# Performance work log

Measured on AMD Instinct MI355X. Metric: run time of the kernel, lower is better.

The kernel has to match this reference:

```python
import jax, jax.numpy as jnp
import numpy as np

B, S, F, H, O = 256, 512, 64, 1024, 24  # batch, seq_len, input_size, hidden_size, output_size


def setup_inputs() -> dict:
    key = jax.random.key(0)
    ks = jax.random.split(key, 11)
    s = 1.0 / np.sqrt(H)  # PyTorch LSTM/Linear uniform init bound
    u = lambda k, shape: jax.random.uniform(k, shape, jnp.float32, -s, s)
    return {
        "x": jax.random.normal(ks[0], (B, S, F), jnp.float32),
        # layer 0 (gate order: i, f, g, o stacked along first dim)
        "W_ih0": u(ks[1], (4 * H, F)),
        "W_hh0": u(ks[2], (4 * H, H)),
        "b_ih0": u(ks[3], (4 * H,)),
        "b_hh0": u(ks[4], (4 * H,)),
        # layer 1
        "W_ih1": u(ks[5], (4 * H, H)),
        "W_hh1": u(ks[6], (4 * H, H)),
        "b_ih1": u(ks[7], (4 * H,)),
        "b_hh1": u(ks[8], (4 * H,)),
        # final projection over all timesteps: [O, H*S]
        "fc_W": jax.random.uniform(ks[9], (O, H * S), jnp.float32, -1.0 / np.sqrt(H * S), 1.0 / np.sqrt(H * S)),
        "fc_b": jax.random.uniform(ks[10], (O,), jnp.float32, -1.0 / np.sqrt(H * S), 1.0 / np.sqrt(H * S)),
    }


def _lstm_layer(x_sbf, W_ih, W_hh, b_ih, b_hh):
    # x_sbf: [S, B, Fin]; returns all hidden states [S, B, H]
    Hh = W_hh.shape[1]
    # precompute input contribution for all steps (one big GEMM)
    xg = jnp.einsum('sbf,gf->sbg', x_sbf, W_ih) + b_ih + b_hh  # [S, B, 4H]

    def step(carry, xg_t):
        h, c = carry
        gates = xg_t + h @ W_hh.T  # [B, 4H]
        i, f, g, o = jnp.split(gates, 4, axis=-1)
        c = jax.nn.sigmoid(f) * c + jax.nn.sigmoid(i) * jnp.tanh(g)
        h = jax.nn.sigmoid(o) * jnp.tanh(c)
        return (h, c), h

    h0 = jnp.zeros((x_sbf.shape[1], Hh), x_sbf.dtype)
    _, hs = jax.lax.scan(step, (h0, h0), xg)
    return hs  # [S, B, H]


def reference(x, W_ih0, W_hh0, b_ih0, b_hh0, W_ih1, W_hh1, b_ih1, b_hh1, fc_W, fc_b):
    xs = jnp.swapaxes(x, 0, 1)  # [S, B, F]
    h1 = _lstm_layer(xs, W_ih0, W_hh0, b_ih0, b_hh0)  # [S, B, H]
    h2 = _lstm_layer(h1, W_ih1, W_hh1, b_ih1, b_hh1)  # [S, B, H]
    # use_all_h=True: reshape [B, S, H] -> [B, S*H], then Linear
    flat = jnp.swapaxes(h2, 0, 1).reshape(x.shape[0], -1)
    return flat @ fc_W.T + fc_b  # [B, O]
```

## Files before the change

kernel.cpp:

```cpp
#include <hip/hip_runtime.h>
#include <hip/hip_fp16.h>

#define B_ 256
#define S_ 512
#define F_ 64
#define H_ 1024
#define O_ 24
#define G_ 4096
#define NT_ 64

typedef _Float16 half_t;
typedef _Float16 h8 __attribute__((ext_vector_type(8)));
typedef float f4 __attribute__((ext_vector_type(4)));

#define OFF_H1 ((size_t)0)
#define OFF_H2 (OFF_H1 + (size_t)2*B_*H_*2)
#define OFF_C1 (OFF_H2 + (size_t)2*B_*H_*2)
#define OFF_C2 (OFF_C1 + (size_t)B_*H_*4)
#define OFF_OP (OFF_C2 + (size_t)B_*H_*4)
#define ZBYTES (OFF_OP + (size_t)NT_*B_*O_*4)
#define OFF_BIAS0 (ZBYTES)
#define OFF_BIAS1 (OFF_BIAS0 + (size_t)G_*4)
#define OFF_XH    (OFF_BIAS1 + (size_t)G_*4)
#define OFF_WIH0  (OFF_XH + (size_t)B_*S_*F_*2)
#define OFF_WHH0  (OFF_WIH0 + (size_t)G_*F_*2)
#define OFF_WIH1  (OFF_WHH0 + (size_t)G_*H_*2)
#define OFF_WHH1  (OFF_WIH1 + (size_t)G_*H_*2)
#define WS_NEEDED (OFF_WHH1 + (size_t)G_*H_*2)

__global__ void k_bias(const float* __restrict__ bi0, const float* __restrict__ bh0,
                       const float* __restrict__ bi1, const float* __restrict__ bh1,
                       float* __restrict__ bias0, float* __restrict__ bias1) {
    int i = blockIdx.x * blockDim.x + threadIdx.x;
    if (i < G_) { bias0[i] = bi0[i] + bh0[i]; bias1[i] = bi1[i] + bh1[i]; }
}

__global__ void k_cvt(const float* __restrict__ src, half_t* __restrict__ dst, int n) {
    int i = blockIdx.x * blockDim.x + threadIdx.x;
    int stride = gridDim.x * blockDim.x;
    for (; i < n; i += stride) dst[i] = (half_t)src[i];
}

__global__ void k_pack(const float* __restrict__ src, half_t* __restrict__ dst, int NC) {
    int i = blockIdx.x * blockDim.x + threadIdx.x;
    int total = 32768 * NC;
    if (i >= total) return;
    int lane = i & 63;
    int j    = (i >> 6) & 3;
    int ck   = (i >> 8) % NC;
    int gh   = i / (256 * NC);
    int srow = (gh >> 5) * H_ + (gh & 31) * 32 + (j >> 1) * 16 + (lane & 15);
    int scol = ck * 64 + (j & 1) * 32 + (lane >> 4) * 8;
    const float* s = src + (size_t)srow * (NC * 64) + scol;
    h8 v;
    #pragma unroll
    for (int e = 0; e < 8; ++e) v[e] = (half_t)s[e];
    *(h8*)&dst[(size_t)i * 8] = v;
}

__device__ __forceinline__ void run_part(
    const int thr, const int bt, const int htp,
    const int cx, const int nchunks,
    const half_t* __restrict__ xb, const int ldx,
    const half_t* __restrict__ hp,
    const half_t* __restrict__ Wih, const half_t* __restrict__ Whh,
    const float* __restrict__ bias,
    float* __restrict__ c, half_t* __restrict__ hn_out,
    const float* __restrict__ fcWt, float* __restrict__ out_part,
    half_t* A_s, float* gate_s, float* h_s, float* fcw_s,
    const bool do_fc)
{
    const int wave = thr >> 6, lane = thr & 63;
    const int gate = wave >> 1, mh = wave & 1;
    const int quad = lane >> 4, l15 = lane & 15;
    const int ar = thr >> 3;
    const int ak = (thr & 7) * 8;
    const int ghW = gate * 32 + (htp >> 1);
    const int jo  = (htp & 1) * 2;

    float bv = bias[gate * H_ + htp * 16 + l15];
    f4 acc0 = (f4){bv, bv, bv, bv};
    f4 acc1 = acc0;

    auto loadA = [&](int ck) -> f4 {
        const half_t* Ab; int lda, k0;
        if (ck < cx) { Ab = xb; lda = ldx; k0 = ck * 64; }
        else         { Ab = hp; lda = H_;  k0 = (ck - cx) * 64; }
        return *(const f4*)&Ab[(size_t)(bt * 64 + ar) * lda + k0 + ak];
    };
    auto fetchW = [&](int ck, h8& r0, h8& r1) {
        const half_t* Wb; int ckk, NC;
        if (ck < cx) { Wb = Wih; ckk = ck;      NC = cx; }
        else         { Wb = Whh; ckk = ck - cx; NC = 16; }
        const half_t* base = Wb + ((size_t)(((ghW * NC) + ckk) * 4 + jo) * 64 + lane) * 8;
        r0 = *(const h8*)(base + 0 * 512);
        r1 = *(const h8*)(base + 1 * 512);
    };

    h8 W0a,W0b, W1a,W1b, W2a,W2b, W3a,W3b;
    f4 p0, p1, p2, p3;
    p0 = loadA(0); p1 = loadA(1); p2 = loadA(2); p3 = loadA(3);
    fetchW(0, W0a, W0b);
    fetchW(1, W1a, W1b);
    fetchW(2, W2a, W2b);

    const int eb = thr >> 4, ecol = thr & 15;
    const size_t cbase = (size_t)(bt * 64 + eb) * H_ + htp * 16 + ecol;
    float cpre0 = c[cbase];
    float cpre1 = c[cbase + (size_t)32 * H_];
    float fpre = 0.f;
    if (do_fc && thr < 384)
        fpre = fcWt[(size_t)(thr >> 4) * (S_ * H_) + htp * 16 + (thr & 15)];

    *(f4*)&A_s[0 * 4608 + ar * 72 + ak] = p0;
    *(f4*)&A_s[1 * 4608 + ar * 72 + ak] = p1;
    *(f4*)&A_s[2 * 4608 + ar * 72 + ak] = p2;
    *(f4*)&A_s[3 * 4608 + ar * 72 + ak] = p3;
    __syncthreads();

    for (int s = 0; s < nchunks; s += 4) {
        const int rem = nchunks - s;
        const int ns = rem < 4 ? rem : 4;
        int ns2 = rem - 4; if (ns2 < 0) ns2 = 0; if (ns2 > 4) ns2 = 4;
        const int bufo = ((s >> 2) & 1) * 18432;
        const int obuf = 18432 - bufo;

        if (ns2 > 0) p0 = loadA(s + 4);
        if (ns2 > 1) p1 = loadA(s + 5);
        if (ns2 > 2) p2 = loadA(s + 6);
        if (ns2 > 3) p3 = loadA(s + 7);

        #define STEP(i, C0,C1, N0,N1)                                                          \
        if (i < ns) {                                                                          \
            if (s + i + 3 < nchunks) fetchW(s + i + 3, N0, N1);                                \
            h8 a0 = *(const h8*)&A_s[bufo + i * 4608 + (mh * 32 + l15) * 72 + quad * 8];       \
            h8 a1 = *(const h8*)&A_s[bufo + i * 4608 + (mh * 32 + 16 + l15) * 72 + quad * 8];  \
            h8 a2 = *(const h8*)&A_s[bufo + i * 4608 + (mh * 32 + l15) * 72 + 32 + quad * 8];  \
            h8 a3 = *(const h8*)&A_s[bufo + i * 4608 + (mh * 32 + 16 + l15) * 72 + 32 + quad * 8]; \
            acc0 = __builtin_amdgcn_mfma_f32_16x16x32_f16(a0, C0, acc0, 0, 0, 0);              \
            acc1 = __builtin_amdgcn_mfma_f32_16x16x32_f16(a1, C0, acc1, 0, 0, 0);              \
            acc0 = __builtin_amdgcn_mfma_f32_16x16x32_f16(a2, C1, acc0, 0, 0, 0);              \
            acc1 = __builtin_amdgcn_mfma_f32_16x16x32_f16(a3, C1, acc1, 0, 0, 0);              \
        }
        STEP(0, W0a,W0b, W3a,W3b)
        STEP(1, W1a,W1b, W0a,W0b)
        STEP(2, W2a,W2b, W1a,W1b)
        STEP(3, W3a,W3b, W2a,W2b)
        #undef STEP

        if (ns2 > 0) {
                   *(f4*)&A_s[obuf + 0 * 4608 + ar * 72 + ak] = p0;
            if (ns2 > 1)     *(f4*)&A_s[obuf + 1 * 4608 + ar * 72 + ak] = p1;
            if (ns2 > 2)     *(f4*)&A_s[obuf + 2 * 4608 + ar * 72 + ak] = p2;
            if (ns2 > 3)     *(f4*)&A_s[obuf + 3 * 4608 + ar * 72 + ak] = p3;
            __syncthreads();
        }
    }
    __syncthreads();

    #pragma unroll
    for (int r = 0; r < 4; ++r) {
        gate_s[gate * (64 * 17) + (mh * 32 + quad * 4 + r) * 17 + l15]      = acc0[r];
        gate_s[gate * (64 * 17) + (mh * 32 + 16 + quad * 4 + r) * 17 + l15] = acc1[r];
    }
    __syncthreads();

    #pragma unroll
    for (int kk = 0; kk < 2; ++kk) {
        int b = eb + kk * 32;
        float gi = gate_s[0 * (64 * 17) + b * 17 + ecol];
        float gf = gate_s[1 * (64 * 17) + b * 17 + ecol];
        float gg = gate_s[2 * (64 * 17) + b * 17 + ecol];
        float go = gate_s[3 * (64 * 17) + b * 17 + ecol];
        float si = 1.f / (1.f + __expf(-gi));
        float sf = 1.f / (1.f + __expf(-gf));
        float so = 1.f / (1.f + __expf(-go));
        float tg = tanhf(gg);
        float cn = sf * (kk ? cpre1 : cpre0) + si * tg;
        size_t cidx = cbase + (size_t)kk * 32 * H_;
        c[cidx] = cn;
        float hnv = so * tanhf(cn);
        hn_out[cidx] = (half_t)hnv;
        if (do_fc) h_s[b * 17 + ecol] = hnv;
    }

    if (do_fc) {
        if (thr < 384) fcw_s[thr] = fpre;
        __syncthreads();
        #pragma unroll
        for (int q = 0; q < 3; ++q) {
            int p = thr + q * 512;
            int o = p >> 6, bb = p & 63;
            float s2 = 0.f;
            #pragma unroll
            for (int j = 0; j < 16; ++j)
                s2 += h_s[bb * 17 + j] * fcw_s[o * 16 + j];
            out_part[(size_t)htp * (B_ * O_) + (bt * 64 + bb) * O_ + o] += s2;
        }
    }
    __syncthreads();
}

__global__ __launch_bounds__(512, 2)
void k_phase(int t,
             const half_t* __restrict__ x_h,
             const half_t* __restrict__ Wih0, const half_t* __restrict__ Whh0,
             const float* __restrict__ bias0, float* __restrict__ c1g, half_t* __restrict__ h1buf,
             const half_t* __restrict__ Wih1, const half_t* __restrict__ Whh1,
             const float* __restrict__ bias1, float* __restrict__ c2g, half_t* __restrict__ h2buf,
             const float* __restrict__ fcW, float* __restrict__ out_part)
{
    __shared__ __align__(16) char smraw[73728];
    half_t* A_s    = (half_t*)smraw;
    float*  gate_s = (float*)smraw;
    float*  h_s    = (float*)(smraw + 17408);
    float*  fcw_s  = (float*)(smraw + 21760);

    const int n   = blockIdx.x;
    const int htp = (n & 7) + 8 * ((n >> 3) & 7);
    const int bt  = (n >> 6) & 3;
    const int thr = threadIdx.x;

    if (t < S_) {
        const int tt = t;
        run_part(thr, bt, htp, 1, 17,
                 x_h + (size_t)tt * F_, S_ * F_,
                 h1buf + (size_t)((tt - 1) & 1) * B_ * H_,
                 Wih0, Whh0, bias0, c1g,
                 h1buf + (size_t)(tt & 1) * B_ * H_,
                 nullptr, nullptr,
                 A_s, gate_s, h_s, fcw_s, false);
    }
    if (t > 0) {
        const int tt = t - 1;
        run_part(thr, bt, htp, 16, 32,
                 h1buf + (size_t)(tt & 1) * B_ * H_, H_,
                 h2buf + (size_t)((tt - 1) & 1) * B_ * H_,
                 Wih1, Whh1, bias1, c2g,
                 h2buf + (size_t)(tt & 1) * B_ * H_,
                 fcW + (size_t)tt * H_, out_part,
                 A_s, gate_s, h_s, fcw_s, true);
    }
}

__global__ void k_final(const float* __restrict__ out_part, const float* __restrict__ fcb,
                        float* __restrict__ out) {
    int i = blockIdx.x * blockDim.x + threadIdx.x;
    if (i >= B_ * O_) return;
    int o = i % O_;
    float s = fcb[o];
    for (int tl = 0; tl < NT_; ++tl) s += out_part[(size_t)tl * (B_ * O_) + i];
    out[i] = s;
}

extern "C" void kernel_launch(void* const* d_in, const int* in_sizes, int n_in,
                              void* d_out, int out_size, void* d_ws, size_t ws_size,
                              hipStream_t stream) {
    const float* x    = (const float*)d_in[0];
    const float* Wih0 = (const float*)d_in[1];
    const float* Whh0 = (const float*)d_in[2];
    const float* bih0 = (const float*)d_in[3];
    const float* bhh0 = (const float*)d_in[4];
    const float* Wih1 = (const float*)d_in[5];
    const float* Whh1 = (const float*)d_in[6];
    const float* bih1 = (const float*)d_in[7];
    const float* bhh1 = (const float*)d_in[8];
    const float* fcW  = (const float*)d_in[9];
    const float* fcb  = (const float*)d_in[10];

    char* ws = (char*)d_ws;
    half_t* h1buf  = (half_t*)(ws + OFF_H1);
    half_t* h2buf  = (half_t*)(ws + OFF_H2);
    float*  c1     = (float*)(ws + OFF_C1);
    float*  c2     = (float*)(ws + OFF_C2);
    float*  opart  = (float*)(ws + OFF_OP);
    float*  bias0  = (float*)(ws + OFF_BIAS0);
    float*  bias1  = (float*)(ws + OFF_BIAS1);
    half_t* x_h    = (half_t*)(ws + OFF_XH);
    half_t* wih0_p = (half_t*)(ws + OFF_WIH0);
    half_t* whh0_p = (half_t*)(ws + OFF_WHH0);
    half_t* wih1_p = (half_t*)(ws + OFF_WIH1);
    half_t* whh1_p = (half_t*)(ws + OFF_WHH1);

    hipMemsetAsync(d_ws, 0, ZBYTES, stream);

    k_bias<<<dim3((G_ + 255) / 256), dim3(256), 0, stream>>>(bih0, bhh0, bih1, bhh1, bias0, bias1);
    k_cvt<<<dim3(2048), dim3(256), 0, stream>>>(x, x_h, B_ * S_ * F_);
    k_pack<<<dim3(128),  dim3(256), 0, stream>>>(Wih0, wih0_p, 1);
    k_pack<<<dim3(2048), dim3(256), 0, stream>>>(Whh0, whh0_p, 16);
    k_pack<<<dim3(2048), dim3(256), 0, stream>>>(Wih1, wih1_p, 16);
    k_pack<<<dim3(2048), dim3(256), 0, stream>>>(Whh1, whh1_p, 16);

    dim3 grid(256), blk(512);
    for (int t = 0; t <= S_; ++t) {
        k_phase<<<grid, blk, 0, stream>>>(t, x_h,
                                          wih0_p, whh0_p, bias0, c1, h1buf,
                                          wih1_p, whh1_p, bias1, c2, h2buf,
                                          fcW, opart);
    }
    k_final<<<dim3((B_ * O_ + 255) / 256), dim3(256), 0, stream>>>(opart, fcb, (float*)d_out);
}
```

Before: 9.640 ms.

## Deepen K-loop prefetch to 8 chunks with doubled weight register pipeline

Restructures the per-step GEMM loop to process 8 K-chunks per iteration. It keeps 7 weight chunks in flight in registers instead of 3, and prefetches A tiles 8 to 12 chunks ahead into two LDS half-buffers. The goal is to hide more global-memory latency in the latency-bound recurrent step. In exchange it roughly doubles the register use for weights and prefetched A, which risks spills or lower occupancy.

```diff
diff --git a/kernel.cpp b/kernel.cpp
--- a/kernel.cpp
+++ b/kernel.cpp
@@ -97,12 +97,20 @@
         r1 = *(const h8*)(base + 1 * 512);
     };
 
-    h8 W0a,W0b, W1a,W1b, W2a,W2b, W3a,W3b;
+    h8 Ws0a,Ws0b, Ws1a,Ws1b, Ws2a,Ws2b, Ws3a,Ws3b,
+       Ws4a,Ws4b, Ws5a,Ws5b, Ws6a,Ws6b, Ws7a{},Ws7b{};
     f4 p0, p1, p2, p3;
-    p0 = loadA(0); p1 = loadA(1); p2 = loadA(2); p3 = loadA(3);
-    fetchW(0, W0a, W0b);
-    fetchW(1, W1a, W1b);
-    fetchW(2, W2a, W2b);
+    f4 q0, q1, q2, q3;
+
+    f4 a0_ = loadA(0), a1_ = loadA(1), a2_ = loadA(2), a3_ = loadA(3);
+    p0 = loadA(4); p1 = loadA(5); p2 = loadA(6); p3 = loadA(7);
+    fetchW(0, Ws0a, Ws0b);
+    fetchW(1, Ws1a, Ws1b);
+    fetchW(2, Ws2a, Ws2b);
+    fetchW(3, Ws3a, Ws3b);
+    fetchW(4, Ws4a, Ws4b);
+    fetchW(5, Ws5a, Ws5b);
+    fetchW(6, Ws6a, Ws6b);
 
     const int eb = thr >> 4, ecol = thr & 15;
     const size_t cbase = (size_t)(bt * 64 + eb) * H_ + htp * 16 + ecol;
@@ -112,51 +120,61 @@
     if (do_fc && thr < 384)
         fpre = fcWt[(size_t)(thr >> 4) * (S_ * H_) + htp * 16 + (thr & 15)];
 
-    *(f4*)&A_s[0 * 4608 + ar * 72 + ak] = p0;
-    *(f4*)&A_s[1 * 4608 + ar * 72 + ak] = p1;
-    *(f4*)&A_s[2 * 4608 + ar * 72 + ak] = p2;
-    *(f4*)&A_s[3 * 4608 + ar * 72 + ak] = p3;
+    *(f4*)&A_s[0 * 4608 + ar * 72 + ak] = a0_;
+    *(f4*)&A_s[1 * 4608 + ar * 72 + ak] = a1_;
+    *(f4*)&A_s[2 * 4608 + ar * 72 + ak] = a2_;
+    *(f4*)&A_s[3 * 4608 + ar * 72 + ak] = a3_;
     __syncthreads();
 
-    for (int s = 0; s < nchunks; s += 4) {
-        const int rem = nchunks - s;
-        const int ns = rem < 4 ? rem : 4;
-        int ns2 = rem - 4; if (ns2 < 0) ns2 = 0; if (ns2 > 4) ns2 = 4;
-        const int bufo = ((s >> 2) & 1) * 18432;
-        const int obuf = 18432 - bufo;
-
-        if (ns2 > 0) p0 = loadA(s + 4);
-        if (ns2 > 1) p1 = loadA(s + 5);
-        if (ns2 > 2) p2 = loadA(s + 6);
-        if (ns2 > 3) p3 = loadA(s + 7);
-
-        #define STEP(i, C0,C1, N0,N1)                                                          \
-        if (i < ns) {                                                                          \
-            if (s + i + 3 < nchunks) fetchW(s + i + 3, N0, N1);                                \
-            h8 a0 = *(const h8*)&A_s[bufo + i * 4608 + (mh * 32 + l15) * 72 + quad * 8];       \
-            h8 a1 = *(const h8*)&A_s[bufo + i * 4608 + (mh * 32 + 16 + l15) * 72 + quad * 8];  \
-            h8 a2 = *(const h8*)&A_s[bufo + i * 4608 + (mh * 32 + l15) * 72 + 32 + quad * 8];  \
-            h8 a3 = *(const h8*)&A_s[bufo + i * 4608 + (mh * 32 + 16 + l15) * 72 + 32 + quad * 8]; \
-            acc0 = __builtin_amdgcn_mfma_f32_16x16x32_f16(a0, C0, acc0, 0, 0, 0);              \
-            acc1 = __builtin_amdgcn_mfma_f32_16x16x32_f16(a1, C0, acc1, 0, 0, 0);              \
-            acc0 = __builtin_amdgcn_mfma_f32_16x16x32_f16(a2, C1, acc0, 0, 0, 0);              \
-            acc1 = __builtin_amdgcn_mfma_f32_16x16x32_f16(a3, C1, acc1, 0, 0, 0);              \
+    for (int s = 0; s < nchunks; s += 8) {
+        if (s + 8  < nchunks) q0 = loadA(s + 8);
+        if (s + 9  < nchunks) q1 = loadA(s + 9);
+        if (s + 10 < nchunks) q2 = loadA(s + 10);
+        if (s + 11 < nchunks) q3 = loadA(s + 11);
+
+        #define STEP(i, C0,C1, N0,N1)                                                            \
+        if (s + i < nchunks) {                                                                   \
+            if (s + i + 7 < nchunks) fetchW(s + i + 7, N0, N1);                                  \
+            const int bo = (i) < 4 ? 0 : 18432;                                                  \
+            const int ii = (i) & 3;                                                              \
+            h8 a0 = *(const h8*)&A_s[bo + ii * 4608 + (mh * 32 + l15) * 72 + quad * 8];          \
+            h8 a1 = *(const h8*)&A_s[bo + ii * 4608 + (mh * 32 + 16 + l15) * 72 + quad * 8];     \
+            h8 a2 = *(const h8*)&A_s[bo + ii * 4608 + (mh * 32 + l15) * 72 + 32 + quad * 8];     \
+            h8 a3 = *(const h8*)&A_s[bo + ii * 4608 + (mh * 32 + 16 + l15) * 72 + 32 + quad * 8];\
+            acc0 = __builtin_amdgcn_mfma_f32_16x16x32_f16(a0, C0, acc0, 0, 0, 0);                \
+            acc1 = __builtin_amdgcn_mfma_f32_16x16x32_f16(a1, C0, acc1, 0, 0, 0);                \
+            acc0 = __builtin_amdgcn_mfma_f32_16x16x32_f16(a2, C1, acc0, 0, 0, 0);                \
+            acc1 = __builtin_amdgcn_mfma_f32_16x16x32_f16(a3, C1, acc1, 0, 0, 0);                \
         }
-        STEP(0, W0a,W0b, W3a,W3b)
-        STEP(1, W1a,W1b, W0a,W0b)
-        STEP(2, W2a,W2b, W1a,W1b)
-        STEP(3, W3a,W3b, W2a,W2b)
+        STEP(0, Ws0a,Ws0b, Ws7a,Ws7b)
+        STEP(1, Ws1a,Ws1b, Ws0a,Ws0b)
+        STEP(2, Ws2a,Ws2b, Ws1a,Ws1b)
+        STEP(3, Ws3a,Ws3b, Ws2a,Ws2b)
+
+        if (s + 4 < nchunks) *(f4*)&A_s[18432 + 0 * 4608 + ar * 72 + ak] = p0;
+        if (s + 5 < nchunks) *(f4*)&A_s[18432 + 1 * 4608 + ar * 72 + ak] = p1;
+        if (s + 6 < nchunks) *(f4*)&A_s[18432 + 2 * 4608 + ar * 72 + ak] = p2;
+        if (s + 7 < nchunks) *(f4*)&A_s[18432 + 3 * 4608 + ar * 72 + ak] = p3;
+
+        if (s + 12 < nchunks) p0 = loadA(s + 12);
+        if (s + 13 < nchunks) p1 = loadA(s + 13);
+        if (s + 14 < nchunks) p2 = loadA(s + 14);
+        if (s + 15 < nchunks) p3 = loadA(s + 15);
+
+        __syncthreads();
+
+        STEP(4, Ws4a,Ws4b, Ws3a,Ws3b)
+        STEP(5, Ws5a,Ws5b, Ws4a,Ws4b)
+        STEP(6, Ws6a,Ws6b, Ws5a,Ws5b)
+        STEP(7, Ws7a,Ws7b, Ws6a,Ws6b)
         #undef STEP
 
-        if (ns2 > 0) {
-                   *(f4*)&A_s[obuf + 0 * 4608 + ar * 72 + ak] = p0;
-            if (ns2 > 1)     *(f4*)&A_s[obuf + 1 * 4608 + ar * 72 + ak] = p1;
-            if (ns2 > 2)     *(f4*)&A_s[obuf + 2 * 4608 + ar * 72 + ak] = p2;
-            if (ns2 > 3)     *(f4*)&A_s[obuf + 3 * 4608 + ar * 72 + ak] = p3;
-            __syncthreads();
-        }
-    }
-    __syncthreads();
+        if (s + 8  < nchunks) *(f4*)&A_s[0 * 4608 + ar * 72 + ak] = q0;
+        if (s + 9  < nchunks) *(f4*)&A_s[1 * 4608 + ar * 72 + ak] = q1;
+        if (s + 10 < nchunks) *(f4*)&A_s[2 * 4608 + ar * 72 + ak] = q2;
+        if (s + 11 < nchunks) *(f4*)&A_s[3 * 4608 + ar * 72 + ak] = q3;
+        __syncthreads();
+    }
 
     #pragma unroll
     for (int r = 0; r < 4; ++r) {
```

Result: slower. 10.26 ms (+6.5%).

## Run several timesteps per launch with a global atomic barrier and register-held state

Applied to the files above, without the earlier changes.

Replaces the one-launch-per-timestep loop with launches that each cover eight timesteps. Blocks synchronise between steps through an atomic-counter grid barrier, and hidden states go into a 9-deep ring buffer. Cell state, biases and FC partial sums now live in registers across the steps and are written back only at the end of each launch, which cuts launch overhead and global c traffic. The approach assumes all 256 blocks are co-resident (launch bounds raised to 4 blocks per CU). Visibility of h across blocks depends on relaxed atomics without explicit fences, which is a correctness risk.

```diff
diff --git a/kernel.cpp b/kernel.cpp
--- a/kernel.cpp
+++ b/kernel.cpp
@@ -8,17 +8,20 @@
 #define O_ 24
 #define G_ 4096
 #define NT_ 64
+#define TPL_ 8
+#define RING_ 9
 
 typedef _Float16 half_t;
 typedef _Float16 h8 __attribute__((ext_vector_type(8)));
 typedef float f4 __attribute__((ext_vector_type(4)));
 
 #define OFF_H1 ((size_t)0)
-#define OFF_H2 (OFF_H1 + (size_t)2*B_*H_*2)
-#define OFF_C1 (OFF_H2 + (size_t)2*B_*H_*2)
+#define OFF_H2 (OFF_H1 + (size_t)RING_*B_*H_*2)
+#define OFF_C1 (OFF_H2 + (size_t)RING_*B_*H_*2)
 #define OFF_C2 (OFF_C1 + (size_t)B_*H_*4)
 #define OFF_OP (OFF_C2 + (size_t)B_*H_*4)
-#define ZBYTES (OFF_OP + (size_t)NT_*B_*O_*4)
+#define OFF_CNT (OFF_OP + (size_t)NT_*B_*O_*4)
+#define ZBYTES (OFF_CNT + 64)
 #define OFF_BIAS0 (ZBYTES)
 #define OFF_BIAS1 (OFF_BIAS0 + (size_t)G_*4)
 #define OFF_XH    (OFF_BIAS1 + (size_t)G_*4)
@@ -58,15 +61,29 @@
     *(h8*)&dst[(size_t)i * 8] = v;
 }
 
+
+__device__ __forceinline__ void gbar(unsigned int* cnt, unsigned int target, int thr) {
+    __syncthreads();
+    if (thr == 0) {
+        asm volatile("" ::: "memory");
+        __hip_atomic_fetch_add(cnt, 1u, __ATOMIC_RELAXED, __HIP_MEMORY_SCOPE_AGENT);
+        while (__hip_atomic_load(cnt, __ATOMIC_RELAXED, __HIP_MEMORY_SCOPE_AGENT) < target)
+            __builtin_amdgcn_s_sleep(4);
+        asm volatile("" ::: "memory");
+    }
+    __syncthreads();
+}
+
 __device__ __forceinline__ void run_part(
     const int thr, const int bt, const int htp,
     const int cx, const int nchunks,
     const half_t* __restrict__ xb, const int ldx,
     const half_t* __restrict__ hp,
     const half_t* __restrict__ Wih, const half_t* __restrict__ Whh,
-    const float* __restrict__ bias,
-    float* __restrict__ c, half_t* __restrict__ hn_out,
-    const float* __restrict__ fcWt, float* __restrict__ out_part,
+    const float bv,
+    float& cpe, float& cpo, half_t* __restrict__ hn_out,
+    const float* __restrict__ fcWt,
+    float& fp0, float& fp1, float& fp2,
     half_t* A_s, float* gate_s, float* h_s, float* fcw_s,
     const bool do_fc)
 {
@@ -78,7 +95,6 @@
     const int ghW = gate * 32 + (htp >> 1);
     const int jo  = (htp & 1) * 2;
 
-    float bv = bias[gate * H_ + htp * 16 + l15];
     f4 acc0 = (f4){bv, bv, bv, bv};
     f4 acc1 = acc0;
 
@@ -99,23 +115,20 @@
 
     h8 W0a,W0b, W1a,W1b, W2a,W2b, W3a,W3b;
     f4 p0, p1, p2, p3;
-    p0 = loadA(0); p1 = loadA(1); p2 = loadA(2); p3 = loadA(3);
+    f4 a0_ = loadA(0), a1_ = loadA(1), a2_ = loadA(2), a3_ = loadA(3);
+    p0 = loadA(4); p1 = loadA(5); p2 = loadA(6); p3 = loadA(7);
     fetchW(0, W0a, W0b);
     fetchW(1, W1a, W1b);
     fetchW(2, W2a, W2b);
 
-    const int eb = thr >> 4, ecol = thr & 15;
-    const size_t cbase = (size_t)(bt * 64 + eb) * H_ + htp * 16 + ecol;
-    float cpre0 = c[cbase];
-    float cpre1 = c[cbase + (size_t)32 * H_];
     float fpre = 0.f;
     if (do_fc && thr < 384)
         fpre = fcWt[(size_t)(thr >> 4) * (S_ * H_) + htp * 16 + (thr & 15)];
 
-    *(f4*)&A_s[0 * 4608 + ar * 72 + ak] = p0;
-    *(f4*)&A_s[1 * 4608 + ar * 72 + ak] = p1;
-    *(f4*)&A_s[2 * 4608 + ar * 72 + ak] = p2;
-    *(f4*)&A_s[3 * 4608 + ar * 72 + ak] = p3;
+    *(f4*)&A_s[0 * 4608 + ar * 72 + ak] = a0_;
+    *(f4*)&A_s[1 * 4608 + ar * 72 + ak] = a1_;
+    *(f4*)&A_s[2 * 4608 + ar * 72 + ak] = a2_;
+    *(f4*)&A_s[3 * 4608 + ar * 72 + ak] = a3_;
     __syncthreads();
 
     for (int s = 0; s < nchunks; s += 4) {
@@ -165,23 +178,32 @@
     }
     __syncthreads();
 
-    #pragma unroll
-    for (int kk = 0; kk < 2; ++kk) {
-        int b = eb + kk * 32;
-        float gi = gate_s[0 * (64 * 17) + b * 17 + ecol];
-        float gf = gate_s[1 * (64 * 17) + b * 17 + ecol];
-        float gg = gate_s[2 * (64 * 17) + b * 17 + ecol];
-        float go = gate_s[3 * (64 * 17) + b * 17 + ecol];
-        float si = 1.f / (1.f + __expf(-gi));
-        float sf = 1.f / (1.f + __expf(-gf));
-        float so = 1.f / (1.f + __expf(-go));
-        float tg = tanhf(gg);
-        float cn = sf * (kk ? cpre1 : cpre0) + si * tg;
-        size_t cidx = cbase + (size_t)kk * 32 * H_;
-        c[cidx] = cn;
-        float hnv = so * tanhf(cn);
-        hn_out[cidx] = (half_t)hnv;
-        if (do_fc) h_s[b * 17 + ecol] = hnv;
+    {
+        const int erow = thr >> 3, ecp = thr & 7;
+        const int c0 = 2 * ecp;
+        float ge = gate_s[0 * (64 * 17) + erow * 17 + c0];
+        float go_ = gate_s[0 * (64 * 17) + erow * 17 + c0 + 1];
+        float fe = gate_s[1 * (64 * 17) + erow * 17 + c0];
+        float fo = gate_s[1 * (64 * 17) + erow * 17 + c0 + 1];
+        float gge = gate_s[2 * (64 * 17) + erow * 17 + c0];
+        float ggo = gate_s[2 * (64 * 17) + erow * 17 + c0 + 1];
+        float oe = gate_s[3 * (64 * 17) + erow * 17 + c0];
+        float oo = gate_s[3 * (64 * 17) + erow * 17 + c0 + 1];
+        float sie = 1.f / (1.f + __expf(-ge)),  sio = 1.f / (1.f + __expf(-go_));
+        float sfe = 1.f / (1.f + __expf(-fe)),  sfo = 1.f / (1.f + __expf(-fo));
+        float soe = 1.f / (1.f + __expf(-oe)),  soo = 1.f / (1.f + __expf(-oo));
+        float tge = tanhf(gge), tgo = tanhf(ggo);
+        float cne = sfe * cpe + sie * tge;
+        float cno = sfo * cpo + sio * tgo;
+        cpe = cne; cpo = cno;
+        float hne = soe * tanhf(cne);
+        float hno = soo * tanhf(cno);
+        union { half_t h[2]; unsigned int u; } cv;
+        cv.h[0] = (half_t)hne; cv.h[1] = (half_t)hno;
+        size_t hidx = (size_t)(bt * 64 + erow) * H_ + htp * 16 + c0;
+        __hip_atomic_store((unsigned int*)&hn_out[hidx], cv.u,
+                           __ATOMIC_RELAXED, __HIP_MEMORY_SCOPE_AGENT);
+        if (do_fc) { h_s[erow * 17 + c0] = hne; h_s[erow * 17 + c0 + 1] = hno; }
     }
 
     if (do_fc) {
@@ -195,20 +217,20 @@
             #pragma unroll
             for (int j = 0; j < 16; ++j)
                 s2 += h_s[bb * 17 + j] * fcw_s[o * 16 + j];
-            out_part[(size_t)htp * (B_ * O_) + (bt * 64 + bb) * O_ + o] += s2;
-        }
-    }
-    __syncthreads();
-}
-
-__global__ __launch_bounds__(512, 2)
-void k_phase(int t,
-             const half_t* __restrict__ x_h,
-             const half_t* __restrict__ Wih0, const half_t* __restrict__ Whh0,
-             const float* __restrict__ bias0, float* __restrict__ c1g, half_t* __restrict__ h1buf,
-             const half_t* __restrict__ Wih1, const half_t* __restrict__ Whh1,
-             const float* __restrict__ bias1, float* __restrict__ c2g, half_t* __restrict__ h2buf,
-             const float* __restrict__ fcW, float* __restrict__ out_part)
+            if (q == 0) fp0 += s2; else if (q == 1) fp1 += s2; else fp2 += s2;
+        }
+    }
+    __syncthreads();
+}
+
+__global__ __launch_bounds__(512, 4)
+void k_mphase(int tbeg, int tcnt, unsigned int* __restrict__ cnt,
+              const half_t* __restrict__ x_h,
+              const half_t* __restrict__ Wih0, const half_t* __restrict__ Whh0,
+              const float* __restrict__ bias0, float* __restrict__ c1g, half_t* __restrict__ h1r,
+              const half_t* __restrict__ Wih1, const half_t* __restrict__ Whh1,
+              const float* __restrict__ bias1, float* __restrict__ c2g, half_t* __restrict__ h2r,
+              const float* __restrict__ fcW, float* __restrict__ out_part)
 {
     __shared__ __align__(16) char smraw[73728];
     half_t* A_s    = (half_t*)smraw;
@@ -220,26 +242,49 @@
     const int htp = (n & 7) + 8 * ((n >> 3) & 7);
     const int bt  = (n >> 6) & 3;
     const int thr = threadIdx.x;
-
-    if (t < S_) {
-        const int tt = t;
-        run_part(thr, bt, htp, 1, 17,
-                 x_h + (size_t)tt * F_, S_ * F_,
-                 h1buf + (size_t)((tt - 1) & 1) * B_ * H_,
-                 Wih0, Whh0, bias0, c1g,
-                 h1buf + (size_t)(tt & 1) * B_ * H_,
-                 nullptr, nullptr,
-                 A_s, gate_s, h_s, fcw_s, false);
-    }
-    if (t > 0) {
-        const int tt = t - 1;
-        run_part(thr, bt, htp, 16, 32,
-                 h1buf + (size_t)(tt & 1) * B_ * H_, H_,
-                 h2buf + (size_t)((tt - 1) & 1) * B_ * H_,
-                 Wih1, Whh1, bias1, c2g,
-                 h2buf + (size_t)(tt & 1) * B_ * H_,
-                 fcW + (size_t)tt * H_, out_part,
-                 A_s, gate_s, h_s, fcw_s, true);
+    const int wave = thr >> 6, lane = thr & 63;
+    const int gate = wave >> 1, l15 = lane & 15;
+
+    const int erow = thr >> 3, ecp = thr & 7;
+    const size_t cb = (size_t)(bt * 64 + erow) * H_ + htp * 16 + 2 * ecp;
+    float c1e = c1g[cb], c1o = c1g[cb + 1];
+    float c2e = c2g[cb], c2o = c2g[cb + 1];
+    float fp0 = 0.f, fp1 = 0.f, fp2 = 0.f;
+    const float bv0 = bias0[gate * H_ + htp * 16 + l15];
+    const float bv1 = bias1[gate * H_ + htp * 16 + l15];
+
+    for (int p = 0; p < tcnt; ++p) {
+        const int t = tbeg + p;
+        if (t < S_) {
+            run_part(thr, bt, htp, 1, 17,
+                     x_h + (size_t)t * F_, S_ * F_,
+                     h1r + (size_t)((t + RING_ - 1) % RING_) * B_ * H_,
+                     Wih0, Whh0, bv0, c1e, c1o,
+                     h1r + (size_t)(t % RING_) * B_ * H_,
+                     nullptr, fp0, fp1, fp2,
+                     A_s, gate_s, h_s, fcw_s, false);
+        }
+        if (t > 0) {
+            const int tt = t - 1;
+            run_part(thr, bt, htp, 16, 32,
+                     h1r + (size_t)(tt % RING_) * B_ * H_, H_,
+                     h2r + (size_t)((tt + RING_ - 1) % RING_) * B_ * H_,
+                     Wih1, Whh1, bv1, c2e, c2o,
+                     h2r + (size_t)(tt % RING_) * B_ * H_,
+                     fcW + (size_t)tt * H_, fp0, fp1, fp2,
+                     A_s, gate_s, h_s, fcw_s, true);
+        }
+        gbar(cnt, 256u * (unsigned)(t + 1), thr);
+    }
+
+    c1g[cb] = c1e; c1g[cb + 1] = c1o;
+    c2g[cb] = c2e; c2g[cb + 1] = c2o;
+    #pragma unroll
+    for (int q = 0; q < 3; ++q) {
+        int p = thr + q * 512;
+        int o = p >> 6, bb = p & 63;
+        size_t oi = (size_t)htp * (B_ * O_) + (bt * 64 + bb) * O_ + o;
+        out_part[oi] += (q == 0 ? fp0 : (q == 1 ? fp1 : fp2));
     }
 }
 
@@ -269,11 +314,12 @@
     const float* fcb  = (const float*)d_in[10];
 
     char* ws = (char*)d_ws;
-    half_t* h1buf  = (half_t*)(ws + OFF_H1);
-    half_t* h2buf  = (half_t*)(ws + OFF_H2);
+    half_t* h1r    = (half_t*)(ws + OFF_H1);
+    half_t* h2r    = (half_t*)(ws + OFF_H2);
     float*  c1     = (float*)(ws + OFF_C1);
     float*  c2     = (float*)(ws + OFF_C2);
     float*  opart  = (float*)(ws + OFF_OP);
+    unsigned int* cnt = (unsigned int*)(ws + OFF_CNT);
     float*  bias0  = (float*)(ws + OFF_BIAS0);
     float*  bias1  = (float*)(ws + OFF_BIAS1);
     half_t* x_h    = (half_t*)(ws + OFF_XH);
@@ -291,12 +337,12 @@
     k_pack<<<dim3(2048), dim3(256), 0, stream>>>(Wih1, wih1_p, 16);
     k_pack<<<dim3(2048), dim3(256), 0, stream>>>(Whh1, whh1_p, 16);
 
-    dim3 grid(256), blk(512);
-    for (int t = 0; t <= S_; ++t) {
-        k_phase<<<grid, blk, 0, stream>>>(t, x_h,
-                                          wih0_p, whh0_p, bias0, c1, h1buf,
-                                          wih1_p, whh1_p, bias1, c2, h2buf,
-                                          fcW, opart);
+    for (int tb = 0; tb <= S_; tb += TPL_) {
+        int tc = S_ + 1 - tb; if (tc > TPL_) tc = TPL_;
+        k_mphase<<<dim3(256), dim3(512), 0, stream>>>(tb, tc, cnt, x_h,
+                                                      wih0_p, whh0_p, bias0, c1, h1r,
+                                                      wih1_p, whh1_p, bias1, c2, h2r,
+                                                      fcW, opart);
     }
     k_final<<<dim3((B_ * O_ + 255) / 256), dim3(256), 0, stream>>>(opart, fcb, (float*)d_out);
 }
```

Result: slower. 14.99 ms (+55.5%).
